# Performance work log

Hardware: AMD Instinct MI355X
Metric: run time of the kernel (lower is better)

Reference implementation:

```python
import jax, jax.numpy as jnp
import numpy as np

B, N, D = 4, 4096, 1024
H, F = 16, 256
HD = D // H
EPS_ATTN = 1e-8
EPS_LN = 1e-5


def setup_inputs() -> dict:
    key = jax.random.key(0)
    ks = jax.random.split(key, 10)
    def kaiming(k, shape):
        fan_in = shape[1]
        return jax.random.normal(k, shape, jnp.float32) * jnp.sqrt(2.0 / fan_in)
    # orthogonal-ish random projection (plain gaussian init, then QR per head)
    pm = jax.random.normal(ks[0], (H, HD, F), jnp.float32)
    return {
        "x": jax.random.normal(ks[1], (B, N, D), jnp.float32),
        "proj": pm,
        "w_qkv": kaiming(ks[2], (3 * D, D)),
        "w_out": kaiming(ks[3], (D, D)),
        "b_out": jnp.zeros((D,), jnp.float32),
        "gamma": jnp.ones((D,), jnp.float32),
        "beta": jnp.zeros((D,), jnp.float32),
        "w1": kaiming(ks[4], (4 * D, D)),
        "b1": jnp.zeros((4 * D,), jnp.float32),
        "w2": kaiming(ks[5], (D, 4 * D)),
        "b2": jnp.zeros((D,), jnp.float32),
    }


def _layernorm(x, gamma, beta):
    mu = jnp.mean(x, axis=-1, keepdims=True)
    var = jnp.var(x, axis=-1, keepdims=True)
    return (x - mu) * jax.lax.rsqrt(var + EPS_LN) * gamma + beta


def reference(x, proj, w_qkv, w_out, b_out, gamma, beta, w1, b1, w2, b2):
    residual = x
    b, n, d = x.shape
    qkv = x @ w_qkv.T                      # (b,n,3d)
    q, k, v = jnp.split(qkv, 3, axis=-1)
    def to_heads(t):
        return t.reshape(b, n, H, HD).transpose(0, 2, 1, 3)  # (b,h,n,hd)
    q, k, v = to_heads(q), to_heads(k), to_heads(v)
    # kernel feature maps: elu(x)+1
    q_f = jax.nn.elu(jnp.einsum('bhnd,hdf->bhnf', q, proj)) + 1.0
    k_f = jax.nn.elu(jnp.einsum('bhnd,hdf->bhnf', k, proj)) + 1.0
    # non-causal FAVOR+ linear attention
    kv = jnp.einsum('bhnf,bhnd->bhfd', k_f, v)               # (b,h,f,hd)
    attn = jnp.einsum('bhnf,bhfd->bhnd', q_f, kv)            # (b,h,n,hd)
    k_sum = jnp.sum(k_f, axis=2)                             # (b,h,f)
    z = 1.0 / (jnp.einsum('bhnf,bhf->bhn', q_f, k_sum) + EPS_ATTN)
    attn = attn * z[..., None]
    attn = attn.transpose(0, 2, 1, 3).reshape(b, n, d)
    x = residual + attn @ w_out.T + b_out
    x = _layernorm(x, gamma, beta)
    h = jax.nn.gelu(x @ w1.T + b1, approximate=False)
    x = x + h @ w2.T + b2
    x = _layernorm(x, gamma, beta)
    return x
```

## Files before the change

kernel.cpp:

```cpp
#include <hip/hip_runtime.h>
#include <math.h>

typedef unsigned short u16;
typedef __bf16 bf16x8 __attribute__((ext_vector_type(8)));
typedef float f32x4 __attribute__((ext_vector_type(4)));
typedef unsigned short u16x4 __attribute__((ext_vector_type(4)));
typedef unsigned short u16x8 __attribute__((ext_vector_type(8)));

#define DEV static __device__ __forceinline__

DEV float bf2f(u16 u) { union { unsigned int i; float f; } x; x.i = ((unsigned int)u) << 16; return x.f; }
DEV u16 f2bf(float f) { union { float f; unsigned int i; } x; x.f = f; unsigned int r = x.i + 0x7fffu + ((x.i >> 16) & 1u); return (u16)(r >> 16); }

DEV void load_lds16(const void* g, void* l) {
  __builtin_amdgcn_global_load_lds((__attribute__((address_space(1))) void*)g,
                                   (__attribute__((address_space(3))) void*)l, 16, 0, 0);
}

DEV float gelu_tanh(float g) {
  float t = 0.7978845608f * g * (1.f + 0.044715f * g * g);
  return g / (1.f + __expf(-2.f * t));
}

template<int EPI>
__global__ __launch_bounds__(256, 2)
void gemm_nt(const u16* __restrict__ A, const u16* __restrict__ B, void* __restrict__ Cv,
             const float* __restrict__ aux0, const void* __restrict__ aux1,
             int M, int N, int K, int lda, int ldb, int ldc)
{
  __shared__ __align__(16) unsigned char smem[32768];
  const int tid = threadIdx.x;
  int bx = blockIdx.x, by = blockIdx.y;
  {
    int nwg = gridDim.x * gridDim.y;
    if ((nwg & 7) == 0) {
      int wg = by * gridDim.x + bx;
      int swz = (wg & 7) * (nwg >> 3) + (wg >> 3);
      bx = swz % gridDim.x; by = swz / gridDim.x;
    }
  }
  const int m0 = by * 128, n0 = bx * 128;
  const int wid = tid >> 6, lane = tid & 63;
  const int wr = wid >> 1, wc = wid & 1;
  const int ln15 = lane & 15, lq = lane >> 4;
  const int srow = tid >> 3, sch = tid & 7;

  f32x4 acc[4][4] = {};

  for (int k0 = 0; k0 < K; k0 += 64) {
#pragma unroll
    for (int i = 0; i < 4; ++i) {
      int r = i * 32 + srow;
      const unsigned char* src = (const unsigned char*)(A + (size_t)(m0 + r) * lda + k0) + ((sch ^ (r & 7)) << 4);
      load_lds16(src, smem + r * 128 + (sch << 4));
    }
#pragma unroll
    for (int i = 0; i < 4; ++i) {
      int r = i * 32 + srow;
      const unsigned char* src = (const unsigned char*)(B + (size_t)(n0 + r) * ldb + k0) + ((sch ^ (r & 7)) << 4);
      load_lds16(src, smem + 16384 + r * 128 + (sch << 4));
    }
    __syncthreads();
#pragma unroll
    for (int kk = 0; kk < 2; ++kk) {
      bf16x8 af[4], bfv[4];
#pragma unroll
      for (int m = 0; m < 4; ++m) {
        int r = wr * 64 + m * 16 + ln15;
        int kc = kk * 4 + lq;
        af[m] = *(const bf16x8*)(smem + r * 128 + ((kc ^ (r & 7)) << 4));
      }
#pragma unroll
      for (int n = 0; n < 4; ++n) {
        int r = wc * 64 + n * 16 + ln15;
        int kc = kk * 4 + lq;
        bfv[n] = *(const bf16x8*)(smem + 16384 + r * 128 + ((kc ^ (r & 7)) << 4));
      }
#pragma unroll
      for (int m = 0; m < 4; ++m)
#pragma unroll
        for (int n = 0; n < 4; ++n)
          acc[m][n] = __builtin_amdgcn_mfma_f32_16x16x32_bf16(af[m], bfv[n], acc[m][n], 0, 0, 0);
    }
    __syncthreads();
  }

#pragma unroll
  for (int m = 0; m < 4; ++m) {
#pragma unroll
    for (int n = 0; n < 4; ++n) {
      int col = n0 + wc * 64 + n * 16 + ln15;
#pragma unroll
      for (int j = 0; j < 4; ++j) {
        int row = m0 + wr * 64 + m * 16 + lq * 4 + j;
        float v = acc[m][n][j];
        size_t idx = (size_t)row * ldc + col;
        if (EPI == 0) {
          ((u16*)Cv)[idx] = f2bf(v);
        } else if (EPI == 3) {
          ((float*)Cv)[idx] = v + aux0[col] + ((const float*)aux1)[idx];
        } else if (EPI == 4) {
          ((u16*)Cv)[idx] = f2bf(gelu_tanh(v + aux0[col]));
        } else if (EPI == 7) {
          ((float*)Cv)[idx] = v + aux0[col] + bf2f(((const u16*)aux1)[idx]);
        }
      }
    }
  }
}

__global__ __launch_bounds__(256, 2)
void fused_kv(const u16* __restrict__ qkv, const u16* __restrict__ projT,
              float* __restrict__ kvpart, float* __restrict__ ksumpart)
{
  __shared__ __align__(16) unsigned char ktS[2][8192];
  __shared__ __align__(16) unsigned char vtS[2][8192];
  __shared__ __align__(16) unsigned char kfS[32768];
  const int tid = threadIdx.x;
  const int bh = blockIdx.y, chunk = blockIdx.x;
  const int b = bh >> 4, h = bh & 15;
  const int wid = tid >> 6, lane = tid & 63;
  const int ln15 = lane & 15, lq = lane >> 4;
  const int vN = tid >> 2, vD = (tid & 3) * 16;
  const int vCn = vN >> 3, vWb = (vN & 7) * 2;

  bf16x8 pf[4][2];
#pragma unroll
  for (int m = 0; m < 4; ++m)
#pragma unroll
    for (int kk = 0; kk < 2; ++kk) {
      int f = wid * 64 + m * 16 + ln15;
      pf[m][kk] = *(const bf16x8*)(projT + (size_t)h * 16384 + (size_t)f * 64 + (kk * 4 + lq) * 8);
    }

  float ksum_r = 0.f;
  f32x4 acc2[4][4] = {};
  const int nbase = chunk * 512;

  {
    const u16* kg = qkv + ((size_t)b * 4096 + nbase) * 3072 + 1024 + h * 64;
#pragma unroll
    for (int i = 0; i < 2; ++i) {
      int c = i * 256 + tid; int r = c >> 3, ch = c & 7;
      load_lds16((const unsigned char*)(kg + (size_t)r * 3072) + ((ch ^ (r & 7)) << 4),
                 ktS[0] + r * 128 + ch * 16);
    }
    const u16* vg = qkv + ((size_t)b * 4096 + nbase + vN) * 3072 + 2048 + h * 64 + vD;
    u16x8 va = *(const u16x8*)vg;
    u16x8 vb = *(const u16x8*)(vg + 8);
#pragma unroll
    for (int j = 0; j < 8; ++j) {
      int d = vD + j;
      *(u16*)(vtS[0] + d * 128 + ((vCn ^ (d & 7)) << 4) + vWb) = va[j];
    }
#pragma unroll
    for (int j = 0; j < 8; ++j) {
      int d = vD + 8 + j;
      *(u16*)(vtS[0] + d * 128 + ((vCn ^ (d & 7)) << 4) + vWb) = vb[j];
    }
  }
  __syncthreads();

  for (int t = 0; t < 8; ++t) {
    const int cur = t & 1, nxt = cur ^ 1;
    u16x8 va, vb;
    const bool havenext = (t + 1 < 8);
    if (havenext) {
      int n1 = nbase + (t + 1) * 64;
      const u16* kg = qkv + ((size_t)b * 4096 + n1) * 3072 + 1024 + h * 64;
#pragma unroll
      for (int i = 0; i < 2; ++i) {
        int c = i * 256 + tid; int r = c >> 3, ch = c & 7;
        load_lds16((const unsigned char*)(kg + (size_t)r * 3072) + ((ch ^ (r & 7)) << 4),
                   ktS[nxt] + r * 128 + ch * 16);
      }
      const u16* vg = qkv + ((size_t)b * 4096 + n1 + vN) * 3072 + 2048 + h * 64 + vD;
      va = *(const u16x8*)vg;
      vb = *(const u16x8*)(vg + 8);
    }

    bf16x8 bvk[2][4];
#pragma unroll
    for (int kk = 0; kk < 2; ++kk)
#pragma unroll
      for (int n = 0; n < 4; ++n) {
        int r = n * 16 + ln15, kc = kk * 4 + lq;
        bvk[kk][n] = *(const bf16x8*)(ktS[cur] + r * 128 + ((kc ^ (r & 7)) << 4));
      }
#pragma unroll
    for (int m = 0; m < 4; ++m) {
      f32x4 a1[4] = {};
#pragma unroll
      for (int kk = 0; kk < 2; ++kk)
#pragma unroll
        for (int n = 0; n < 4; ++n)
          a1[n] = __builtin_amdgcn_mfma_f32_16x16x32_bf16(pf[m][kk], bvk[kk][n], a1[n], 0, 0, 0);
#pragma unroll
      for (int n = 0; n < 4; ++n) {
        int nloc = n * 16 + ln15;
        int c = nloc >> 3, wb = (nloc & 7) * 2;
#pragma unroll
        for (int j = 0; j < 4; ++j) {
          int f = wid * 64 + m * 16 + lq * 4 + j;
          float v = a1[n][j];
          float o = v > 0.f ? v + 1.f : __expf(v);
          *(u16*)(kfS + f * 128 + ((c ^ (f & 7)) << 4) + wb) = f2bf(o);
        }
      }
    }
    __syncthreads();

    {
      int f = tid;
      float s = 0.f;
#pragma unroll
      for (int c = 0; c < 8; ++c) {
        u16x8 v = *(const u16x8*)(kfS + f * 128 + ((c ^ (f & 7)) << 4));
#pragma unroll
        for (int j = 0; j < 8; ++j) s += bf2f(v[j]);
      }
      ksum_r += s;
    }
#pragma unroll
    for (int kk = 0; kk < 2; ++kk) {
      int kc = kk * 4 + lq;
      bf16x8 af[4], bv[4];
#pragma unroll
      for (int m = 0; m < 4; ++m) { int r = wid * 64 + m * 16 + ln15; af[m] = *(const bf16x8*)(kfS + r * 128 + ((kc ^ (r & 7)) << 4)); }
#pragma unroll
      for (int n = 0; n < 4; ++n) { int r = n * 16 + ln15; bv[n] = *(const bf16x8*)(vtS[cur] + r * 128 + ((kc ^ (r & 7)) << 4)); }
#pragma unroll
      for (int m = 0; m < 4; ++m)
#pragma unroll
        for (int n = 0; n < 4; ++n)
          acc2[m][n] = __builtin_amdgcn_mfma_f32_16x16x32_bf16(af[m], bv[n], acc2[m][n], 0, 0, 0);
    }
    if (havenext) {
#pragma unroll
      for (int j = 0; j < 8; ++j) {
        int d = vD + j;
        *(u16*)(vtS[nxt] + d * 128 + ((vCn ^ (d & 7)) << 4) + vWb) = va[j];
      }
#pragma unroll
      for (int j = 0; j < 8; ++j) {
        int d = vD + 8 + j;
        *(u16*)(vtS[nxt] + d * 128 + ((vCn ^ (d & 7)) << 4) + vWb) = vb[j];
      }
    }
    __syncthreads();
  }

  const size_t pbase = ((size_t)bh * 8 + chunk) * 16384;
#pragma unroll
  for (int half = 0; half < 2; ++half) {
#pragma unroll
    for (int m = 0; m < 4; ++m)
#pragma unroll
      for (int n2 = 0; n2 < 2; ++n2) {
        int n = half * 2 + n2;
        int dloc = n2 * 16 + ln15;
        int f = wid * 64 + m * 16 + lq * 4;
        *(f32x4*)(kfS + dloc * 1024 + ((f * 4) ^ ((dloc & 7) << 4))) = acc2[m][n];
      }
    __syncthreads();
#pragma unroll
    for (int k = 0; k < 8; ++k) {
      int dloc = k * 4 + wid;
      f32x4 val = *(const f32x4*)(kfS + dloc * 1024 + ((lane * 16) ^ ((dloc & 7) << 4)));
      *(f32x4*)(kvpart + pbase + (size_t)(half * 32 + dloc) * 256 + lane * 4) = val;
    }
    __syncthreads();
  }
  ksumpart[((size_t)bh * 8 + chunk) * 256 + tid] = ksum_r;
}

__global__ __launch_bounds__(256) void kv_finalize(const float* __restrict__ kvpart,
    const float* __restrict__ ksumpart, u16* __restrict__ kvT, float* __restrict__ ksum)
{
  int bx = blockIdx.x, bh = bx >> 2, dq = bx & 3, tid = threadIdx.x;
  const float* base = kvpart + (size_t)bh * 131072;
  u16* out = kvT + (size_t)bh * 16384;
#pragma unroll
  for (int k = 0; k < 16; ++k) {
    int idx = dq * 4096 + k * 256 + tid;
    float s = 0.f;
#pragma unroll
    for (int c = 0; c < 8; ++c) s += base[(size_t)c * 16384 + idx];
    out[idx] = f2bf(s);
  }
  if (dq == 0) {
    float s = 0.f;
#pragma unroll
    for (int c = 0; c < 8; ++c) s += ksumpart[((size_t)bh * 8 + c) * 256 + tid];
    ksum[(size_t)bh * 256 + tid] = s;
  }
}

__global__ __launch_bounds__(256, 3)
void fused_attn(const u16* __restrict__ qkv, const u16* __restrict__ projT,
                const u16* __restrict__ kvT, const float* __restrict__ ksum,
                u16* __restrict__ attnb)
{
  __shared__ __align__(16) unsigned char qtS[8192];
  __shared__ __align__(16) unsigned char qfS[32768];
  __shared__ float zpart[64][4];
  __shared__ float zS[64];
  const int tid = threadIdx.x;
  const int bh = blockIdx.y, nt = blockIdx.x;
  const int b = bh >> 4, h = bh & 15;
  const int wid = tid >> 6, lane = tid & 63;
  const int ln15 = lane & 15, lq = lane >> 4;
  const int n0 = nt * 64;

  bf16x8 pf[4][2];
#pragma unroll
  for (int n = 0; n < 4; ++n)
#pragma unroll
    for (int kk = 0; kk < 2; ++kk) {
      int f = wid * 64 + n * 16 + ln15;
      pf[n][kk] = *(const bf16x8*)(projT + (size_t)h * 16384 + (size_t)f * 64 + (kk * 4 + lq) * 8);
    }

  const u16* qg = qkv + ((size_t)b * 4096 + n0) * 3072 + h * 64;
#pragma unroll
  for (int i = 0; i < 2; ++i) {
    int c = i * 256 + tid; int r = c >> 3, ch = c & 7;
    load_lds16((const unsigned char*)(qg + (size_t)r * 3072) + ((ch ^ (r & 7)) << 4),
               qtS + r * 128 + ch * 16);
  }
  __syncthreads();

#pragma unroll
  for (int m = 0; m < 4; ++m) {
    bf16x8 af[2];
#pragma unroll
    for (int kk = 0; kk < 2; ++kk) {
      int r = m * 16 + ln15, kc = kk * 4 + lq;
      af[kk] = *(const bf16x8*)(qtS + r * 128 + ((kc ^ (r & 7)) << 4));
    }
    f32x4 a1[4] = {};
#pragma unroll
    for (int kk = 0; kk < 2; ++kk)
#pragma unroll
      for (int n = 0; n < 4; ++n)
        a1[n] = __builtin_amdgcn_mfma_f32_16x16x32_bf16(af[kk], pf[n][kk], a1[n], 0, 0, 0);
#pragma unroll
    for (int n = 0; n < 4; ++n) {
      int f = wid * 64 + n * 16 + ln15;
      int c = f >> 3, wb = (f & 7) * 2;
#pragma unroll
      for (int j = 0; j < 4; ++j) {
        int row = m * 16 + lq * 4 + j;
        float v = a1[n][j];
        float o = v > 0.f ? v + 1.f : __expf(v);
        *(u16*)(qfS + row * 512 + ((c ^ (row & 7)) << 4) + wb) = f2bf(o);
      }
    }
  }
  __syncthreads();

  {
    int n = tid & 63, q = tid >> 6;
    const float* kp = ksum + (size_t)bh * 256;
    float s = 0.f;
#pragma unroll
    for (int c = q * 8; c < q * 8 + 8; ++c) {
      u16x8 v = *(const u16x8*)(qfS + n * 512 + ((c ^ (n & 7)) << 4));
#pragma unroll
      for (int j = 0; j < 8; ++j) s += bf2f(v[j]) * kp[c * 8 + j];
    }
    zpart[n][q] = s;
  }
  __syncthreads();
  if (tid < 64) zS[tid] = 1.f / (zpart[tid][0] + zpart[tid][1] + zpart[tid][2] + zpart[tid][3] + 1e-8f);
  __syncthreads();

  f32x4 a2[4] = {};
  const u16* kvg = kvT + (size_t)bh * 16384;
#pragma unroll
  for (int kk = 0; kk < 8; ++kk) {
    int kc = kk * 4 + lq;
    int r = wid * 16 + ln15;
    bf16x8 af = *(const bf16x8*)(qfS + r * 512 + ((kc ^ (r & 7)) << 4));
#pragma unroll
    for (int nf = 0; nf < 4; ++nf) {
      int d = nf * 16 + ln15;
      bf16x8 bv = *(const bf16x8*)(kvg + (size_t)d * 256 + kc * 8);
      a2[nf] = __builtin_amdgcn_mfma_f32_16x16x32_bf16(af, bv, a2[nf], 0, 0, 0);
    }
  }
#pragma unroll
  for (int nf = 0; nf < 4; ++nf)
#pragma unroll
    for (int j = 0; j < 4; ++j) {
      int d = nf * 16 + ln15;
      int n = wid * 16 + lq * 4 + j;
      float v = a2[nf][j] * zS[n];
      attnb[((size_t)b * 4096 + n0 + n) * 1024 + h * 64 + d] = f2bf(v);
    }
}

__global__ __launch_bounds__(256) void cast_kernel(const float* __restrict__ in, u16* __restrict__ out, int n4)
{
  int i = blockIdx.x * 256 + threadIdx.x;
  if (i >= n4) return;
  float4 v = ((const float4*)in)[i];
  u16x4 o = { f2bf(v.x), f2bf(v.y), f2bf(v.z), f2bf(v.w) };
  ((u16x4*)out)[i] = o;
}

__global__ __launch_bounds__(256) void projt_kernel(const float* __restrict__ proj, u16* __restrict__ out)
{
  int i = blockIdx.x * 256 + threadIdx.x;
  int d = i & 63, f = (i >> 6) & 255, h = i >> 14;
  out[i] = f2bf(proj[((size_t)h * 64 + d) * 256 + f]);
}

__global__ __launch_bounds__(256) void ln_kernel(const float* __restrict__ in, const float* __restrict__ gamma,
                                                 const float* __restrict__ beta, float* __restrict__ outF,
                                                 u16* __restrict__ outB)
{
  int row = blockIdx.x, tid = threadIdx.x;
  float4 v = ((const float4*)(in + (size_t)row * 1024))[tid];
  float s = v.x + v.y + v.z + v.w;
  float q = v.x * v.x + v.y * v.y + v.z * v.z + v.w * v.w;
  for (int off = 32; off; off >>= 1) { s += __shfl_down(s, off); q += __shfl_down(q, off); }
  __shared__ float rs[4], rq[4];
  int wid = tid >> 6, lane = tid & 63;
  if (!lane) { rs[wid] = s; rq[wid] = q; }
  __syncthreads();
  s = rs[0] + rs[1] + rs[2] + rs[3];
  q = rq[0] + rq[1] + rq[2] + rq[3];
  float mu = s * (1.f / 1024.f);
  float rstd = rsqrtf(q * (1.f / 1024.f) - mu * mu + 1e-5f);
  float4 g = ((const float4*)gamma)[tid];
  float4 bb = ((const float4*)beta)[tid];
  float4 o;
  o.x = (v.x - mu) * rstd * g.x + bb.x;
  o.y = (v.y - mu) * rstd * g.y + bb.y;
  o.z = (v.z - mu) * rstd * g.z + bb.z;
  o.w = (v.w - mu) * rstd * g.w + bb.w;
  if (outF) ((float4*)(outF + (size_t)row * 1024))[tid] = o;
  if (outB) {
    u16x4 ob = { f2bf(o.x), f2bf(o.y), f2bf(o.z), f2bf(o.w) };
    ((u16x4*)(outB + (size_t)row * 1024))[tid] = ob;
  }
}

#define O_WQKVB   0L
#define O_WOUTB   6291456L
#define O_W1B     8388608L
#define O_W2B     16777216L
#define O_PROJT   25165824L
#define O_KSUM    25690112L
#define O_KSP     26804224L
#define O_KVB     27852800L
#define O_QFG     37289984L
#define O_QKVB    70844416L
#define O_ATTNB   171507712L
#define WS_NEED   205062144L

extern "C" void kernel_launch(void* const* d_in, const int* in_sizes, int n_in,
                              void* d_out, int out_size, void* d_ws, size_t ws_size,
                              hipStream_t stream)
{
  if (ws_size < (size_t)WS_NEED) return;

  const float* x     = (const float*)d_in[0];
  const float* proj  = (const float*)d_in[1];
  const float* wqkv  = (const float*)d_in[2];
  const float* wout  = (const float*)d_in[3];
  const float* bout  = (const float*)d_in[4];
  const float* gamma = (const float*)d_in[5];
  const float* beta  = (const float*)d_in[6];
  const float* w1    = (const float*)d_in[7];
  const float* b1    = (const float*)d_in[8];
  const float* w2    = (const float*)d_in[9];
  const float* b2    = (const float*)d_in[10];
  float* outp = (float*)d_out;
  char* ws = (char*)d_ws;

  u16* wqkvb  = (u16*)(ws + O_WQKVB);
  u16* woutb  = (u16*)(ws + O_WOUTB);
  u16* w1b    = (u16*)(ws + O_W1B);
  u16* w2b    = (u16*)(ws + O_W2B);
  u16* projTb = (u16*)(ws + O_PROJT);
  float* ksumf= (float*)(ws + O_KSUM);
  float* ksp  = (float*)(ws + O_KSP);
  u16* kvTb   = (u16*)(ws + O_KVB);
  u16* qkvb   = (u16*)(ws + O_QKVB);
  u16* attnb  = (u16*)(ws + O_ATTNB);
  u16* x1b    = (u16*)(ws + O_QFG);
  u16* hfull  = (u16*)(ws + O_QKVB);

  u16* xbD   = (u16*)d_out;
  float* kvp = (float*)d_out;

  cast_kernel<<<16384, 256, 0, stream>>>(x, xbD, 4194304);
  cast_kernel<<<3072, 256, 0, stream>>>(wqkv, wqkvb, 786432);
  cast_kernel<<<1024, 256, 0, stream>>>(wout, woutb, 262144);
  cast_kernel<<<4096, 256, 0, stream>>>(w1, w1b, 1048576);
  cast_kernel<<<4096, 256, 0, stream>>>(w2, w2b, 1048576);
  projt_kernel<<<1024, 256, 0, stream>>>(proj, projTb);

  gemm_nt<0><<<dim3(24, 128), 256, 0, stream>>>(xbD, wqkvb, qkvb, nullptr, nullptr,
      16384, 3072, 1024, 1024, 1024, 3072);

  fused_kv<<<dim3(8, 64), 256, 0, stream>>>(qkvb, projTb, kvp, ksp);
  kv_finalize<<<256, 256, 0, stream>>>(kvp, ksp, kvTb, ksumf);
  fused_attn<<<dim3(64, 64), 256, 0, stream>>>(qkvb, projTb, kvTb, ksumf, attnb);

  gemm_nt<3><<<dim3(8, 128), 256, 0, stream>>>(attnb, woutb, outp, bout, x,
      16384, 1024, 1024, 1024, 1024, 1024);

  ln_kernel<<<16384, 256, 0, stream>>>(outp, gamma, beta, nullptr, x1b);

  gemm_nt<4><<<dim3(32, 128), 256, 0, stream>>>(x1b, w1b, hfull, b1, nullptr,
      16384, 4096, 1024, 1024, 1024, 4096);

  gemm_nt<7><<<dim3(8, 128), 256, 0, stream>>>(hfull, w2b, outp, b2, x1b,
      16384, 1024, 4096, 4096, 4096, 1024);

  ln_kernel<<<16384, 256, 0, stream>>>(outp, gamma, beta, outp, nullptr);
}
```

Measured before the change: 696.7 us.

## Tile-group workgroup swizzle per XCD, merge weight casts, read bf16 residual

```diff
diff --git a/kernel.cpp b/kernel.cpp
--- a/kernel.cpp
+++ b/kernel.cpp
@@ -32,11 +32,22 @@
   const int tid = threadIdx.x;
   int bx = blockIdx.x, by = blockIdx.y;
   {
-    int nwg = gridDim.x * gridDim.y;
+    const int GX = gridDim.x;
+    const int nwg = GX * gridDim.y;
     if ((nwg & 7) == 0) {
-      int wg = by * gridDim.x + bx;
-      int swz = (wg & 7) * (nwg >> 3) + (wg >> 3);
-      bx = swz % gridDim.x; by = swz / gridDim.x;
+      const int wg = by * GX + bx;
+      const int cpx = nwg >> 3;
+      const int xcd = wg & 7, s = wg >> 3;
+      const int rows = cpx / GX;
+      if ((GX & 7) == 0 && cpx == rows * GX && (rows & 7) == 0) {
+        const int SC = GX >> 3;
+        const int q = s >> 6, r = (s >> 3) & 7, c = s & 7;
+        by = xcd * rows + (q / SC) * 8 + r;
+        bx = (q % SC) * 8 + c;
+      } else {
+        const int swz = xcd * cpx + s;
+        bx = swz % GX; by = swz / GX;
+      }
     }
   }
   const int m0 = by * 128, n0 = bx * 128;
@@ -407,6 +418,23 @@
   float4 v = ((const float4*)in)[i];
   u16x4 o = { f2bf(v.x), f2bf(v.y), f2bf(v.z), f2bf(v.w) };
   ((u16x4*)out)[i] = o;
+}
+
+__global__ __launch_bounds__(256) void castw_kernel(const float* __restrict__ wqkv, const float* __restrict__ wout,
+                                                    const float* __restrict__ w1, const float* __restrict__ w2,
+                                                    u16* __restrict__ owqkv, u16* __restrict__ owout,
+                                                    u16* __restrict__ ow1, u16* __restrict__ ow2)
+{
+  int bid = blockIdx.x;
+  const float* src; u16* dst; int base;
+  if (bid < 3072)      { src = wqkv; dst = owqkv; base = bid; }
+  else if (bid < 4096) { src = wout; dst = owout; base = bid - 3072; }
+  else if (bid < 8192) { src = w1;   dst = ow1;   base = bid - 4096; }
+  else                 { src = w2;   dst = ow2;   base = bid - 8192; }
+  int i = base * 256 + threadIdx.x;
+  float4 v = ((const float4*)src)[i];
+  u16x4 o = { f2bf(v.x), f2bf(v.y), f2bf(v.z), f2bf(v.w) };
+  ((u16x4*)dst)[i] = o;
 }
 
 __global__ __launch_bounds__(256) void projt_kernel(const float* __restrict__ proj, u16* __restrict__ out)
@@ -488,19 +516,17 @@
   float* ksumf= (float*)(ws + O_KSUM);
   float* ksp  = (float*)(ws + O_KSP);
   u16* kvTb   = (u16*)(ws + O_KVB);
+  float* kvp  = (float*)(ws + O_QFG);
+  u16* x1b    = (u16*)(ws + O_QFG);
   u16* qkvb   = (u16*)(ws + O_QKVB);
+  float* tf   = (float*)(ws + O_QKVB);
+  u16* hfull  = (u16*)(ws + O_QKVB);
   u16* attnb  = (u16*)(ws + O_ATTNB);
-  u16* x1b    = (u16*)(ws + O_QFG);
-  u16* hfull  = (u16*)(ws + O_QKVB);
-
-  u16* xbD   = (u16*)d_out;
-  float* kvp = (float*)d_out;
+
+  u16* xbD = (u16*)d_out;
 
   cast_kernel<<<16384, 256, 0, stream>>>(x, xbD, 4194304);
-  cast_kernel<<<3072, 256, 0, stream>>>(wqkv, wqkvb, 786432);
-  cast_kernel<<<1024, 256, 0, stream>>>(wout, woutb, 262144);
-  cast_kernel<<<4096, 256, 0, stream>>>(w1, w1b, 1048576);
-  cast_kernel<<<4096, 256, 0, stream>>>(w2, w2b, 1048576);
+  castw_kernel<<<12288, 256, 0, stream>>>(wqkv, wout, w1, w2, wqkvb, woutb, w1b, w2b);
   projt_kernel<<<1024, 256, 0, stream>>>(proj, projTb);
 
   gemm_nt<0><<<dim3(24, 128), 256, 0, stream>>>(xbD, wqkvb, qkvb, nullptr, nullptr,
@@ -510,10 +536,10 @@
   kv_finalize<<<256, 256, 0, stream>>>(kvp, ksp, kvTb, ksumf);
   fused_attn<<<dim3(64, 64), 256, 0, stream>>>(qkvb, projTb, kvTb, ksumf, attnb);
 
-  gemm_nt<3><<<dim3(8, 128), 256, 0, stream>>>(attnb, woutb, outp, bout, x,
+  gemm_nt<7><<<dim3(8, 128), 256, 0, stream>>>(attnb, woutb, tf, bout, xbD,
       16384, 1024, 1024, 1024, 1024, 1024);
 
-  ln_kernel<<<16384, 256, 0, stream>>>(outp, gamma, beta, nullptr, x1b);
+  ln_kernel<<<16384, 256, 0, stream>>>(tf, gamma, beta, nullptr, x1b);
 
   gemm_nt<4><<<dim3(32, 128), 256, 0, stream>>>(x1b, w1b, hfull, b1, nullptr,
       16384, 4096, 1024, 1024, 1024, 4096);
```

After: 656.8 us. 5.7% less time.
